# Performance work log

Measured on AMD Instinct MI355X. Metric: run time of the kernel, lower is better.

Reference implementation:

```python
import jax, jax.numpy as jnp
import numpy as np

EPS = 1e-5
DILATIONS = (1, 2, 1, 2, 1, 2, 1, 2)   # 4 blocks x 2 layers, kernel_size=2
GCN_AT = {1: 0, 5: 1}                  # ChebConv applied before layers 1 and 5
N_NODES, T_IN, N_EDGES = 20000, 13, 200000
RC, DC, SC, EC, HORIZON = 32, 32, 256, 512, 12


def conv_1x1(x, W, b):
    # x: [N,C,T], W: [O,C] -> [N,O,T]
    return jnp.einsum('oc,nct->not', W, x) + b[None, :, None]


def conv_k2(x, W, b, d):
    # dilated conv, kernel=2, dilation=d. x: [N,C,T], W: [O,C,2] -> [N,O,T-d]
    y = jnp.einsum('oc,nct->not', W[:, :, 0], x[:, :, :-d]) \
        + jnp.einsum('oc,nct->not', W[:, :, 1], x[:, :, d:])
    return y + b[None, :, None]


def _batchnorm(x):
    # BatchNorm2d (train mode, gamma=1, beta=0); per-channel stats over (N, F=1, T)
    m = jnp.mean(x, axis=(0, 2), keepdims=True)
    v = jnp.var(x, axis=(0, 2), keepdims=True)
    return (x - m) / jnp.sqrt(v + EPS)


def _cheb(xf, edge_index, edge_attr, W0, W1, b):
    n = xf.shape[0]
    row, col = edge_index[0], edge_index[1]
    w = jnp.where(row == col, 0.0, edge_attr)               # remove_self_loops
    deg = jax.ops.segment_sum(w, row, num_segments=n)
    dinv = jnp.where(deg > 0, 1.0 / jnp.sqrt(jnp.where(deg > 0, deg, 1.0)), 0.0)
    norm = dinv[row] * w * dinv[col]                        # [E]
    tx1 = -jax.ops.segment_sum(norm[:, None] * xf[row], col, num_segments=n)
    return xf @ W0 + tx1 @ W1 + b


def _forward(x, edge_index, edge_attr, start_W, start_b, filter_W, filter_b,
             gate_W, gate_b, skip_W, skip_b, gcn0_W0, gcn0_W1, gcn0_b,
             gcn1_W0, gcn1_W1, gcn1_b, end1_W, end1_b, end2_W, end2_b):
    # instance norm over time (use_norm=True); means is detached in torch
    means = jax.lax.stop_gradient(jnp.mean(x, axis=1, keepdims=True))   # [N,1,1]
    xc = x - means
    stdev = jnp.sqrt(jnp.var(xc, axis=1, keepdims=True) + EPS)
    xc = xc / stdev
    h = xc[:, :, 0][:, None, :]                  # [N,1,13]  (F=1 dim folded away)
    h = conv_1x1(h, start_W, start_b)            # [N,32,13]; T == receptive_field, no pad
    gcns = ((gcn0_W0, gcn0_W1, gcn0_b), (gcn1_W0, gcn1_W1, gcn1_b))
    skip = None
    for i, d in enumerate(DILATIONS):
        if i in GCN_AT:
            n, c, t = h.shape
            W0, W1, b = gcns[GCN_AT[i]]
            h = _cheb(h.reshape(n, c * t), edge_index, edge_attr, W0, W1, b).reshape(n, c, t)
        residual = h
        f = jnp.tanh(conv_k2(residual, filter_W[i], filter_b[i], d))
        g = jax.nn.sigmoid(conv_k2(residual, gate_W[i], gate_b[i], d))
        h = f * g                                 # [N,32,t-d]
        s = conv_1x1(h, skip_W[i], skip_b[i])     # [N,256,t-d]
        skip = s if skip is None else s + skip[:, :, -s.shape[2]:]
        h = h + residual[:, :, -h.shape[2]:]      # residual add (residual_conv unused in source)
        h = _batchnorm(h)
    out = jax.nn.relu(skip)                       # [N,256,1]
    out = conv_1x1(out, end1_W, end1_b)           # [N,512,1]
    out = conv_1x1(out, end2_W, end2_b)           # [N,12,1]
    return out * stdev + means                    # de-normalize; broadcasts over horizon


def setup_inputs() -> dict:
    key = jax.random.key(0)
    ks = iter(jax.random.split(key, 32))
    def w(shape, scale=0.1):
        return jax.random.normal(next(ks), shape, dtype=jnp.float32) * scale
    return {
        'x': jax.random.normal(next(ks), (N_NODES, T_IN, 1), dtype=jnp.float32),
        'edge_index': jax.random.randint(next(ks), (2, N_EDGES), 0, N_NODES),
        'edge_attr': jax.random.uniform(next(ks), (N_EDGES,), dtype=jnp.float32),
        'start_W': w((RC, 1)), 'start_b': w((RC,)),
        'filter_W': w((8, DC, RC, 2)), 'filter_b': w((8, DC)),
        'gate_W': w((8, DC, RC, 2)), 'gate_b': w((8, DC)),
        'skip_W': w((8, SC, DC)), 'skip_b': w((8, SC)),
        'gcn0_W0': w((384, 384), 0.05), 'gcn0_W1': w((384, 384), 0.05), 'gcn0_b': w((384,)),
        'gcn1_W0': w((192, 192), 0.05), 'gcn1_W1': w((192, 192), 0.05), 'gcn1_b': w((192,)),
        'end1_W': w((EC, SC)), 'end1_b': w((EC,)),
        'end2_W': w((HORIZON, EC)), 'end2_b': w((HORIZON,)),
    }


def reference(x, edge_index, edge_attr, start_W, start_b, filter_W, filter_b,
              gate_W, gate_b, skip_W, skip_b, gcn0_W0, gcn0_W1, gcn0_b,
              gcn1_W0, gcn1_W1, gcn1_b, end1_W, end1_b, end2_W, end2_b):
    return _forward(x, edge_index, edge_attr, start_W, start_b, filter_W, filter_b,
                    gate_W, gate_b, skip_W, skip_b, gcn0_W0, gcn0_W1, gcn0_b,
                    gcn1_W0, gcn1_W1, gcn1_b, end1_W, end1_b, end2_W, end2_b)
```

## Files before the change

### kernel.cpp

```cpp
#include <hip/hip_runtime.h>
#include <math.h>

#define NN 20000
#define NE 200000
#define TT 13
#define NBLK 79

typedef short bf16x8 __attribute__((ext_vector_type(8)));
typedef float f32x4 __attribute__((ext_vector_type(4)));

__device__ inline unsigned short f2bf(float f){
  union{float f; unsigned u;} v; v.f = f;
  unsigned r = v.u + 0x7fffu + ((v.u >> 16) & 1u);
  return (unsigned short)(r >> 16);
}
__device__ inline float bf2f(unsigned short h){
  union{unsigned u; float f;} v; v.u = ((unsigned)h) << 16; return v.f;
}
__device__ inline float fsig(float x){ return __builtin_amdgcn_rcpf(1.f + __expf(-x)); }
__device__ inline float ftanh(float x){ return 2.f*__builtin_amdgcn_rcpf(1.f + __expf(-2.f*x)) - 1.f; }

__global__ __launch_bounds__(256) void k_instnorm(const float* __restrict__ x,
    float* __restrict__ xc, float* __restrict__ stdev, float* __restrict__ means){
  int n = blockIdx.x*256 + threadIdx.x;
  if(n >= NN) return;
  float v[TT]; float s = 0.f;
#pragma unroll
  for(int t=0;t<TT;t++){ v[t] = x[n*TT+t]; s += v[t]; }
  float m = s * (1.0f/TT);
  float s2 = 0.f;
#pragma unroll
  for(int t=0;t<TT;t++){ v[t] -= m; s2 += v[t]*v[t]; }
  float sd = sqrtf(s2*(1.0f/TT) + 1e-5f);
  float inv = 1.0f/sd;
#pragma unroll
  for(int t=0;t<TT;t++) xc[n*TT+t] = v[t]*inv;
  stdev[n] = sd; means[n] = m;
}

__global__ __launch_bounds__(256) void k_start2(const float* __restrict__ xc,
    const float* __restrict__ sW, const float* __restrict__ sb, unsigned short* __restrict__ h){
  int idx = blockIdx.x*256 + threadIdx.x;
  if(idx >= NN*TT*16) return;
  int cp = idx & 15; int t = (idx >> 4) % TT; int n = idx/(16*TT);
  float xv = xc[n*TT+t];
  int c0 = cp*2;
  unsigned u = (unsigned)f2bf(sW[c0]*xv + sb[c0]) | ((unsigned)f2bf(sW[c0+1]*xv + sb[c0+1]) << 16);
  *(unsigned*)(h + (size_t)n*TT*32 + t*32 + c0) = u;
}

__global__ __launch_bounds__(256) void k_deg(const int* __restrict__ ei,
    const float* __restrict__ ea, float* __restrict__ deg){
  int e = blockIdx.x*256 + threadIdx.x;
  if(e >= NE) return;
  int r = ei[e], c = ei[NE+e];
  float w = (r==c) ? 0.f : ea[e];
  if(w != 0.f) atomicAdd(&deg[r], w);
}

__global__ __launch_bounds__(256) void k_dinv(float* __restrict__ deg){
  int n = blockIdx.x*256 + threadIdx.x;
  if(n >= NN) return;
  float d = deg[n];
  deg[n] = (d > 0.f) ? rsqrtf(d) : 0.f;
}

__global__ __launch_bounds__(256) void k_normcount(const int* __restrict__ ei,
    const float* __restrict__ ea, const float* __restrict__ dinv,
    float* __restrict__ nrm, int* __restrict__ cnt){
  int e = blockIdx.x*256 + threadIdx.x;
  if(e >= NE) return;
  int r = ei[e], c = ei[NE+e];
  float w = (r==c) ? 0.f : ea[e];
  float nv = dinv[r]*w*dinv[c];
  nrm[e] = nv;
  if(nv != 0.f) atomicAdd(&cnt[c], 1);
}

__global__ __launch_bounds__(256) void k_scanA(const int* __restrict__ cnt, int* __restrict__ bsum){
  int i = blockIdx.x*256 + threadIdx.x;
  int l = threadIdx.x & 63, w = threadIdx.x >> 6;
  int v = (i < NN) ? cnt[i] : 0;
#pragma unroll
  for(int off = 1; off < 64; off <<= 1) v += __shfl_xor(v, off);
  __shared__ int ws4[4];
  if(l == 0) ws4[w] = v;
  __syncthreads();
  if(threadIdx.x == 0) bsum[blockIdx.x] = ws4[0]+ws4[1]+ws4[2]+ws4[3];
}

__global__ __launch_bounds__(128) void k_scanB(const int* __restrict__ bsum, int* __restrict__ bbase){
  __shared__ int buf[128];
  int t = threadIdx.x;
  int v = (t < NBLK) ? bsum[t] : 0;
  buf[t] = v; __syncthreads();
  for(int off = 1; off < 128; off <<= 1){
    int u = (t >= off) ? buf[t-off] : 0;
    __syncthreads();
    buf[t] += u;
    __syncthreads();
  }
  if(t < NBLK) bbase[t] = buf[t] - v;
  if(t == NBLK-1) bbase[NBLK] = buf[t];
}

__global__ __launch_bounds__(256) void k_scanC(const int* __restrict__ cnt,
    const int* __restrict__ bbase, int* __restrict__ rowptr, int* __restrict__ woff){
  int i = blockIdx.x*256 + threadIdx.x;
  int t = threadIdx.x, l = t & 63, w = t >> 6;
  int v = (i < NN) ? cnt[i] : 0;
  int x = v;
#pragma unroll
  for(int off = 1; off < 64; off <<= 1){
    int u = __shfl_up(x, off);
    if(l >= off) x += u;
  }
  __shared__ int wt[4];
  if(l == 63) wt[w] = x;
  __syncthreads();
  int wo = 0;
  for(int k = 0; k < w; k++) wo += wt[k];
  int excl = bbase[blockIdx.x] + wo + x - v;
  if(i < NN){ rowptr[i] = excl; woff[i] = excl; }
  if(i == 0) rowptr[NN] = bbase[NBLK];
}

__global__ __launch_bounds__(256) void k_place(const float* __restrict__ nrm,
    const int* __restrict__ ei, int* __restrict__ woff,
    int* __restrict__ rowArr, float* __restrict__ nrmArr){
  int e = blockIdx.x*256 + threadIdx.x;
  if(e >= NE) return;
  float nv = nrm[e];
  if(nv == 0.f) return;
  int c = ei[NE+e];
  int pos = atomicAdd(&woff[c], 1);
  rowArr[pos] = ei[e];
  nrmArr[pos] = nv;
}

__global__ __launch_bounds__(64) void k_bnfold(const float* __restrict__ in, float* __restrict__ out){
  int t = threadIdx.x;
  float s = 0.f;
#pragma unroll
  for(int b = 0; b < 16; b++) s += in[b*64 + t];
  out[t] = s;
}

__device__ inline void d_prepw2(const float* W0, const float* W1, const float* b,
    unsigned short* Wt, float* bPerm, int F, int Kp, int T, int idx){
  if(idx >= F*Kp) return;
  int o = idx / Kp, k = idx - o*Kp;
  int to = o >> 5, co = o & 31; int fout = co*T + to;
  int ki = (k < F) ? k : k - F;
  int ti = ki >> 5, ci = ki & 31; int fin = ci*T + ti;
  float v = (k < F) ? W0[fin*F + fout] : W1[fin*F + fout];
  Wt[idx] = f2bf(v);
  if(k == 0) bPerm[o] = b[fout];
}
__device__ inline void d_prep2(const float* sW, const float* sb,
    unsigned short* Bwt, float* b2, int idx){
  if(idx >= 65536) return;
  int sOut = idx >> 8; int ic = idx & 255; int i = ic >> 5; int c = ic & 31;
  Bwt[idx] = f2bf(sW[i*8192 + sOut*32 + c]);
  if(idx < 256){
    float acc = 0.f;
    for(int ll = 0; ll < 8; ll++) acc += sb[ll*256 + idx];
    b2[idx] = acc;
  }
}
__device__ inline void d_comb(const float* e1W, const float* e1b,
    const float* e2W, const float* e2b, float* Wc, float* bc, int idx){
  if(idx >= 12*256) return;
  int k = idx >> 8, c = idx & 255;
  float acc = 0.f;
  for(int o = 0; o < 512; o++) acc += e2W[k*512+o]*e1W[o*256+c];
  Wc[idx] = acc;
  if(c == 0){
    float b = e2b[k];
    for(int o = 0; o < 512; o++) b += e2W[k*512+o]*e1b[o];
    bc[k] = b;
  }
}
__device__ inline void d_prepg(const float* fW, const float* fb,
    const float* gW, const float* gb, unsigned short* Wfrag, float* Bfrag, int idx){
  if(idx < 8*8*64*8){
    int j = idx & 7; int lane = (idx >> 3) & 63; int chunk = (idx >> 9) & 7; int layer = idx >> 12;
    int fg = chunk >> 2; int q = (chunk >> 1) & 1; int i = chunk & 1;
    int quad = lane >> 4, tcol = lane & 15;
    int cout = 16*i + tcol, cin = quad*8 + j;
    const float* W = fg ? gW : fW;
    Wfrag[idx] = f2bf(W[layer*2048 + cout*64 + cin*2 + q]);
  }
  if(idx < 8*64*4){
    int r = idx & 3; int lane = (idx >> 2) & 63; int layer = idx >> 8;
    int tcol = lane & 15;
    float v;
    if(r == 0)      v = fb[layer*32 + tcol];
    else if(r == 1) v = fb[layer*32 + 16 + tcol];
    else if(r == 2) v = gb[layer*32 + tcol];
    else            v = gb[layer*32 + 16 + tcol];
    Bfrag[idx] = v;
  }
}
__global__ __launch_bounds__(256) void k_prepall(
    const float* g0W0, const float* g0W1, const float* g0b,
    const float* g1W0, const float* g1W1, const float* g1b,
    const float* sW, const float* sb,
    const float* e1W, const float* e1b, const float* e2W, const float* e2b,
    const float* fW, const float* fb, const float* gW, const float* gb,
    unsigned short* Wt0, float* bP0, unsigned short* Wt1, float* bP1,
    unsigned short* Bwt, float* bias2, float* Wc, float* bc,
    unsigned short* Wfrag, float* Bfrag){
  int b = blockIdx.x, t = threadIdx.x;
  if(b < 1152)       d_prepw2(g0W0, g0W1, g0b, Wt0, bP0, 384, 768, 12, b*256 + t);
  else if(b < 1440)  d_prepw2(g1W0, g1W1, g1b, Wt1, bP1, 192, 384, 6, (b-1152)*256 + t);
  else if(b < 1696)  d_prep2(sW, sb, Bwt, bias2, (b-1440)*256 + t);
  else if(b < 1708)  d_comb(e1W, e1b, e2W, e2b, Wc, bc, (b-1696)*256 + t);
  else               d_prepg(fW, fb, gW, gb, Wfrag, Bfrag, (b-1708)*256 + t);
}

__global__ __launch_bounds__(256) void k_cvtbn2(const unsigned short* __restrict__ h,
    const float* __restrict__ bn, float cntInv, unsigned short* __restrict__ A,
    int F, int Kp){
  int idx = blockIdx.x*256 + threadIdx.x;
  int half = F >> 1;
  if(idx >= NN*half) return;
  int n = idx / half, r = idx - n*half;
  int k0 = 2*r; int c0 = k0 & 31;
  unsigned u = *(const unsigned*)(h + (size_t)n*F + k0);
  float m0 = bn[c0]*cntInv, m1 = bn[c0+1]*cntInv;
  float i0 = rsqrtf(bn[32+c0]*cntInv - m0*m0 + 1e-5f);
  float i1 = rsqrtf(bn[32+c0+1]*cntInv - m1*m1 + 1e-5f);
  float v0 = (bf2f((unsigned short)(u & 0xffffu)) - m0)*i0;
  float v1 = (bf2f((unsigned short)(u >> 16)) - m1)*i1;
  unsigned outw = (unsigned)f2bf(v0) | ((unsigned)f2bf(v1) << 16);
  *(unsigned*)(A + (size_t)n*Kp + k0) = outw;
}

__global__ void k_gather2(const unsigned short* __restrict__ Acat, int Kp, int F, int F2,
    const int* __restrict__ rowArr, const float* __restrict__ nrmArr,
    const int* __restrict__ rowptr, unsigned short* __restrict__ dst){
  int node = blockIdx.x;
  int f2 = threadIdx.x;
  int beg = rowptr[node], end = rowptr[node+1];
  __shared__ int srow[64];
  __shared__ float snrm[64];
  float a0 = 0.f, a1 = 0.f;
  for(int base = beg; base < end; base += 64){
    int m = end - base; if(m > 64) m = 64;
    __syncthreads();
    if(threadIdx.x < m){ srow[threadIdx.x] = rowArr[base+threadIdx.x]; snrm[threadIdx.x] = nrmArr[base+threadIdx.x]; }
    __syncthreads();
    if(f2 < F2){
      for(int j = 0; j < m; j++){
        unsigned u = *(const unsigned*)(Acat + (size_t)srow[j]*Kp + 2*f2);
        float nv = snrm[j];
        a0 += nv*bf2f((unsigned short)(u & 0xffffu));
        a1 += nv*bf2f((unsigned short)(u >> 16));
      }
    }
  }
  if(f2 < F2){
    unsigned outw = (unsigned)f2bf(-a0) | ((unsigned)f2bf(-a1) << 16);
    *(unsigned*)(dst + (size_t)node*Kp + F + 2*f2) = outw;
  }
}

template<bool BOUT>
__global__ __launch_bounds__(256) void k_gemm_bf16(const unsigned short* __restrict__ A,
    const unsigned short* __restrict__ Bt, const float* __restrict__ bias,
    void* __restrict__ Cv, int M, int N, int K){
  __shared__ unsigned short As[128*32];
  __shared__ unsigned short Bs[64*32];
  int tid = threadIdx.x;
  int w = tid >> 6, l = tid & 63, quad = l >> 4, tcol = l & 15;
  int m0 = blockIdx.x*128, n0 = blockIdx.y*64;
  int rw = (w & 1)*64, cw = (w >> 1)*32;
  int sr = tid >> 2, sc = (tid & 3)*8;
  f32x4 acc[4][2];
#pragma unroll
  for(int i=0;i<4;i++)
#pragma unroll
    for(int j=0;j<2;j++) acc[i][j] = (f32x4){0.f,0.f,0.f,0.f};
  for(int k0 = 0; k0 < K; k0 += 32){
    uint4 a0 = *(const uint4*)(A + (size_t)(m0 + sr)*K + k0 + sc);
    uint4 a1 = *(const uint4*)(A + (size_t)(m0 + 64 + sr)*K + k0 + sc);
    uint4 b0 = *(const uint4*)(Bt + (size_t)(n0 + sr)*K + k0 + sc);
    __syncthreads();
    *(uint4*)(As + sr*32 + sc) = a0;
    *(uint4*)(As + (64+sr)*32 + sc) = a1;
    *(uint4*)(Bs + sr*32 + sc) = b0;
    __syncthreads();
    bf16x8 av[4], bv[2];
#pragma unroll
    for(int i=0;i<4;i++) av[i] = *(const bf16x8*)(As + (rw + 16*i + tcol)*32 + quad*8);
#pragma unroll
    for(int j=0;j<2;j++) bv[j] = *(const bf16x8*)(Bs + (cw + 16*j + tcol)*32 + quad*8);
#pragma unroll
    for(int i=0;i<4;i++)
#pragma unroll
      for(int j=0;j<2;j++)
        acc[i][j] = __builtin_amdgcn_mfma_f32_16x16x32_bf16(av[i], bv[j], acc[i][j], 0, 0, 0);
  }
#pragma unroll
  for(int i=0;i<4;i++){
#pragma unroll
    for(int j=0;j<2;j++){
      int col = n0 + cw + 16*j + tcol;
      float bb = bias[col];
#pragma unroll
      for(int r=0;r<4;r++){
        int row = m0 + rw + 16*i + quad*4 + r;
        if(row < M){
          float o = acc[i][j][r] + bb;
          if(BOUT) ((unsigned short*)Cv)[(size_t)row*N + col] = f2bf(o);
          else ((float*)Cv)[(size_t)row*N + col] = o;
        }
      }
    }
  }
}

template<int D,int TIN,int TOUT,bool BNIN,bool STATS,bool WRITEH>
__global__ __launch_bounds__(256) void k_gated5(
    const unsigned short* __restrict__ hIn, unsigned short* __restrict__ hOut,
    unsigned short* __restrict__ gl,
    const float* __restrict__ bnIn, float* __restrict__ bnOut,
    const unsigned short* __restrict__ Wfrag, const float* __restrict__ Bfrag,
    int layer, float cntInv){
  constexpr int RS = 40;
  __shared__ unsigned short hs[4][2][TIN*RS];
  __shared__ unsigned short ho[4][2][WRITEH ? TOUT*RS : RS];
  __shared__ float bnm[32], bnv[32];
  __shared__ float bnred[64];
  int tid = threadIdx.x;
  int w = tid >> 6, l = tid & 63, quad = l >> 4, tcol = l & 15;
  if(BNIN && tid < 32){
    float s = 0.f, s2 = 0.f;
#pragma unroll
    for(int b = 0; b < 16; b++){ s += bnIn[b*64 + tid]; s2 += bnIn[b*64 + 32 + tid]; }
    float m = s*cntInv;
    float var = s2*cntInv - m*m;
    bnm[tid] = m; bnv[tid] = rsqrtf(var + 1e-5f);
  }
  if(STATS && tid < 64) bnred[tid] = 0.f;
  __syncthreads();
  float sm[8], sv[8];
  if(BNIN){
    int cb = (l & 3)*8;
#pragma unroll
    for(int j=0;j<8;j++){ sm[j] = bnm[cb+j]; sv[j] = bnv[cb+j]; }
  }
  const unsigned short* wfr = Wfrag + layer*4096;
  bf16x8 bwf[2][2], bwg[2][2];
#pragma unroll
  for(int q=0;q<2;q++)
#pragma unroll
    for(int i=0;i<2;i++){
      bwf[q][i] = *(const bf16x8*)(wfr + ((q*2+i)*64 + l)*8);
      bwg[q][i] = *(const bf16x8*)(wfr + ((4 + q*2+i)*64 + l)*8);
    }
  float4 bv4 = *(const float4*)(Bfrag + layer*256 + l*4);
  float fbv[2] = {bv4.x, bv4.y}, gbv[2] = {bv4.z, bv4.w};

  int tr = (tcol < TOUT) ? tcol : 0;
  unsigned short* hwA = hs[w][0];
  unsigned short* hwB = hs[w][1];
  unsigned short* howA = ho[w][0];
  unsigned short* howB = ho[w][1];
  float sA[2] = {0.f,0.f}, s2A[2] = {0.f,0.f};
  int wid = blockIdx.x*4 + w;
  int base = wid*8;
  bool ldact = (l < TIN*4);
  int ts = l >> 2, cb = (l & 3)*8;
  uint4 vA = {0,0,0,0}, vB = {0,0,0,0};
  if(ldact && base < NN){
    vA = *(const uint4*)(hIn + (size_t)base*TIN*32 + l*8);
    vB = *(const uint4*)(hIn + (size_t)(base+1)*TIN*32 + l*8);
  }
  for(int p = 0; p < 4; p++){
    int nA = base + 2*p;
    if(nA >= NN) break;
    int nB = nA + 1;
    if(ldact){
      if(BNIN){
        unsigned short tA[8], tB[8];
        const unsigned short* uA = (const unsigned short*)&vA;
        const unsigned short* uB = (const unsigned short*)&vB;
#pragma unroll
        for(int j=0;j<8;j++){
          tA[j] = f2bf((bf2f(uA[j]) - sm[j])*sv[j]);
          tB[j] = f2bf((bf2f(uB[j]) - sm[j])*sv[j]);
        }
        *(uint4*)(hwA + ts*RS + cb) = *(const uint4*)tA;
        *(uint4*)(hwB + ts*RS + cb) = *(const uint4*)tB;
      } else {
        *(uint4*)(hwA + ts*RS + cb) = vA;
        *(uint4*)(hwB + ts*RS + cb) = vB;
      }
    }
    if(p < 3 && ldact && nA + 2 < NN){
      vA = *(const uint4*)(hIn + (size_t)(nA+2)*TIN*32 + l*8);
      vB = *(const uint4*)(hIn + (size_t)(nA+3)*TIN*32 + l*8);
    }
    bf16x8 aA0 = *(const bf16x8*)(hwA + tr*RS + quad*8);
    bf16x8 aA1 = *(const bf16x8*)(hwA + (tr+D)*RS + quad*8);
    bf16x8 aB0 = *(const bf16x8*)(hwB + tr*RS + quad*8);
    bf16x8 aB1 = *(const bf16x8*)(hwB + (tr+D)*RS + quad*8);
    f32x4 afA[2], agA[2], afB[2], agB[2];
#pragma unroll
    for(int i=0;i<2;i++){
      afA[i] = (f32x4){0.f,0.f,0.f,0.f}; agA[i] = afA[i];
      afB[i] = afA[i]; agB[i] = afA[i];
    }
#pragma unroll
    for(int i=0;i<2;i++){
      afA[i] = __builtin_amdgcn_mfma_f32_16x16x32_bf16(aA0, bwf[0][i], afA[i], 0,0,0);
      afB[i] = __builtin_amdgcn_mfma_f32_16x16x32_bf16(aB0, bwf[0][i], afB[i], 0,0,0);
      afA[i] = __builtin_amdgcn_mfma_f32_16x16x32_bf16(aA1, bwf[1][i], afA[i], 0,0,0);
      afB[i] = __builtin_amdgcn_mfma_f32_16x16x32_bf16(aB1, bwf[1][i], afB[i], 0,0,0);
      agA[i] = __builtin_amdgcn_mfma_f32_16x16x32_bf16(aA0, bwg[0][i], agA[i], 0,0,0);
      agB[i] = __builtin_amdgcn_mfma_f32_16x16x32_bf16(aB0, bwg[0][i], agB[i], 0,0,0);
      agA[i] = __builtin_amdgcn_mfma_f32_16x16x32_bf16(aA1, bwg[1][i], agA[i], 0,0,0);
      agB[i] = __builtin_amdgcn_mfma_f32_16x16x32_bf16(aB1, bwg[1][i], agB[i], 0,0,0);
    }
#pragma unroll
    for(int i=0;i<2;i++){
      int cout = 16*i + tcol;
#pragma unroll
      for(int r=0;r<4;r++){
        int t = quad*4 + r;
        if(t < TOUT){
          float fA = afA[i][r] + fbv[i];
          float gA = agA[i][r] + gbv[i];
          float fB = afB[i][r] + fbv[i];
          float gB = agB[i][r] + gbv[i];
          float gatedA = ftanh(fA)*fsig(gA);
          float gatedB = ftanh(fB)*fsig(gB);
          if(t == TOUT-1){
            gl[(size_t)nA*256 + cout] = f2bf(gatedA);
            gl[(size_t)nB*256 + cout] = f2bf(gatedB);
          }
          float oA = gatedA + bf2f(hwA[(t+D)*RS + cout]);
          float oB = gatedB + bf2f(hwB[(t+D)*RS + cout]);
          if(WRITEH){ howA[t*RS + cout] = f2bf(oA); howB[t*RS + cout] = f2bf(oB); }
          if(STATS){ sA[i] += oA + oB; s2A[i] += oA*oA + oB*oB; }
        }
      }
    }
    if(WRITEH && l < TOUT*4){
      int to = l >> 2, cb2 = (l & 3)*8;
      *(uint4*)(hOut + (size_t)nA*TOUT*32 + to*32 + cb2) = *(const uint4*)(howA + to*RS + cb2);
      *(uint4*)(hOut + (size_t)nB*TOUT*32 + to*32 + cb2) = *(const uint4*)(howB + to*RS + cb2);
    }
  }
  if(STATS){
#pragma unroll
    for(int i=0;i<2;i++){
      sA[i]  += __shfl_xor(sA[i], 16);  sA[i]  += __shfl_xor(sA[i], 32);
      s2A[i] += __shfl_xor(s2A[i], 16); s2A[i] += __shfl_xor(s2A[i], 32);
    }
    if(l < 16){
#pragma unroll
      for(int i=0;i<2;i++){
        atomicAdd(&bnred[16*i + l], sA[i]);
        atomicAdd(&bnred[32 + 16*i + l], s2A[i]);
      }
    }
    __syncthreads();
    if(tid < 64) atomicAdd(&bnOut[(blockIdx.x & 15)*64 + tid], bnred[tid]);
  }
}

__global__ __launch_bounds__(256) void k_final(const float* __restrict__ skip,
    const float* __restrict__ Wc, const float* __restrict__ bc,
    const float* __restrict__ stdev, const float* __restrict__ means,
    float* __restrict__ out){
  __shared__ float wsm[3072];
  __shared__ float bcs[12];
  int tid = threadIdx.x;
  for(int j = tid; j < 3072; j += 256){
    int c = j / 12, k = j - c*12;
    wsm[c*12 + k] = Wc[k*256 + c];
  }
  if(tid < 12) bcs[tid] = bc[tid];
  __syncthreads();
  int idx = blockIdx.x*256 + tid;
  if(idx >= NN*12) return;
  int n = idx / 12, k = idx - n*12;
  const float* sr = skip + (size_t)n*256;
  float acc = bcs[k];
#pragma unroll 8
  for(int c = 0; c < 256; c++) acc += wsm[c*12 + k]*fmaxf(sr[c], 0.f);
  out[idx] = acc*stdev[n] + means[n];
}

extern "C" void kernel_launch(void* const* d_in, const int* in_sizes, int n_in,
                              void* d_out, int out_size, void* d_ws, size_t ws_size,
                              hipStream_t stream) {
  const float* x      = (const float*)d_in[0];
  const int*   ei     = (const int*)  d_in[1];
  const float* ea     = (const float*)d_in[2];
  const float* startW = (const float*)d_in[3];
  const float* startb = (const float*)d_in[4];
  const float* fW     = (const float*)d_in[5];
  const float* fb     = (const float*)d_in[6];
  const float* gW     = (const float*)d_in[7];
  const float* gb     = (const float*)d_in[8];
  const float* sW     = (const float*)d_in[9];
  const float* sb     = (const float*)d_in[10];
  const float* g0W0   = (const float*)d_in[11];
  const float* g0W1   = (const float*)d_in[12];
  const float* g0b    = (const float*)d_in[13];
  const float* g1W0   = (const float*)d_in[14];
  const float* g1W1   = (const float*)d_in[15];
  const float* g1b    = (const float*)d_in[16];
  const float* e1W    = (const float*)d_in[17];
  const float* e1b    = (const float*)d_in[18];
  const float* e2W    = (const float*)d_in[19];
  const float* e2b    = (const float*)d_in[20];
  float* out = (float*)d_out;
  float* ws  = (float*)d_ws;

  const int MP = 20096;
  size_t o = 0;
  unsigned short* hA = (unsigned short*)(ws + o); o += (size_t)NN*208;
  unsigned short* hB = (unsigned short*)(ws + o); o += (size_t)NN*208;
  unsigned short* Acat  = (unsigned short*)(ws + o); o += (size_t)MP*384;
  unsigned short* glcat = (unsigned short*)(ws + o); o += (size_t)MP*128;
  unsigned short* Wt0 = (unsigned short*)(ws + o); o += 147456;
  unsigned short* Wt1 = (unsigned short*)(ws + o); o += 36864;
  unsigned short* Bwt = (unsigned short*)(ws + o); o += 32768;
  unsigned short* Wfrag = (unsigned short*)(ws + o); o += 16384;
  float* Bfrag = ws + o; o += 2048;
  float* bP0   = ws + o; o += 384;
  float* bP1   = ws + o; o += 192;
  float* bias2 = ws + o; o += 256;
  float* Wc    = ws + o; o += 3072;
  float* bc    = ws + o; o += 16;
  float* stdev = ws + o; o += NN;
  float* means = ws + o; o += NN;
  float* xc    = ws + o; o += (size_t)NN*TT;
  float* deg   = ws + o; o += NN;
  int*   cnt   = (int*)(ws + o); o += NN;
  float* bnstats = ws + o; o += 8*1024;
  float* bnf0  = ws + o; o += 64;
  float* bnf1  = ws + o; o += 64;
  float* normb = ws + o; o += NE;
  int*   rowArr = (int*)(ws + o); o += NE;
  float* nrmArr = ws + o; o += NE;
  int*   rowptr = (int*)(ws + o); o += NN + 4;
  int*   woff   = (int*)(ws + o); o += NN;
  int*   bsum   = (int*)(ws + o); o += NBLK + 4;
  int*   bbase  = (int*)(ws + o); o += NBLK + 4;
  float* skipb  = (float*)hA;

  hipMemsetAsync(deg, 0, (2*NN + 8*1024)*sizeof(float), stream);
  k_instnorm<<<(NN+255)/256, 256, 0, stream>>>(x, xc, stdev, means);
  k_start2<<<((NN*TT*16)+255)/256, 256, 0, stream>>>(xc, startW, startb, hA);
  k_deg<<<(NE+255)/256, 256, 0, stream>>>(ei, ea, deg);
  k_dinv<<<(NN+255)/256, 256, 0, stream>>>(deg);
  k_normcount<<<(NE+255)/256, 256, 0, stream>>>(ei, ea, deg, normb, cnt);
  k_scanA<<<NBLK, 256, 0, stream>>>(cnt, bsum);
  k_scanB<<<1, 128, 0, stream>>>(bsum, bbase);
  k_scanC<<<NBLK, 256, 0, stream>>>(cnt, bbase, rowptr, woff);
  k_place<<<(NE+255)/256, 256, 0, stream>>>(normb, ei, woff, rowArr, nrmArr);
  k_prepall<<<1836, 256, 0, stream>>>(g0W0, g0W1, g0b, g1W0, g1W1, g1b,
      sW, sb, e1W, e1b, e2W, e2b, fW, fb, gW, gb,
      Wt0, bP0, Wt1, bP1, Bwt, bias2, Wc, bc, Wfrag, Bfrag);

  const int GB = 640;
  k_gated5<1,13,12,false,true,true><<<GB,256,0,stream>>>(hA, hB, glcat+0,
      bnstats, bnstats+0*1024, Wfrag, Bfrag, 0, 0.f);
  k_bnfold<<<1, 64, 0, stream>>>(bnstats+0*1024, bnf0);
  k_cvtbn2<<<((NN*192)+255)/256, 256, 0, stream>>>(hB, bnf0, 1.f/(NN*12.f), Acat, 384, 768);
  k_gather2<<<NN, 192, 0, stream>>>(Acat, 768, 384, 192, rowArr, nrmArr, rowptr, Acat);
  { dim3 g(MP/128, 384/64);
    k_gemm_bf16<true><<<g, 256, 0, stream>>>(Acat, Wt0, bP0, hA, NN, 384, 768); }
  k_gated5<2,12,10,false,true,true><<<GB,256,0,stream>>>(hA, hB, glcat+32,
      bnstats, bnstats+1*1024, Wfrag, Bfrag, 1, 0.f);
  k_gated5<1,10,9,true,true,true><<<GB,256,0,stream>>>(hB, hA, glcat+64,
      bnstats+1*1024, bnstats+2*1024, Wfrag, Bfrag, 2, 1.f/(NN*10.f));
  k_gated5<2,9,7,true,true,true><<<GB,256,0,stream>>>(hA, hB, glcat+96,
      bnstats+2*1024, bnstats+3*1024, Wfrag, Bfrag, 3, 1.f/(NN*9.f));
  k_gated5<1,7,6,true,true,true><<<GB,256,0,stream>>>(hB, hA, glcat+128,
      bnstats+3*1024, bnstats+4*1024, Wfrag, Bfrag, 4, 1.f/(NN*7.f));
  k_bnfold<<<1, 64, 0, stream>>>(bnstats+4*1024, bnf1);
  k_cvtbn2<<<((NN*96)+255)/256, 256, 0, stream>>>(hA, bnf1, 1.f/(NN*6.f), Acat, 192, 384);
  k_gather2<<<NN, 128, 0, stream>>>(Acat, 384, 192, 96, rowArr, nrmArr, rowptr, Acat);
  { dim3 g(MP/128, 192/64);
    k_gemm_bf16<true><<<g, 256, 0, stream>>>(Acat, Wt1, bP1, hB, NN, 192, 384); }
  k_gated5<2,6,4,false,true,true><<<GB,256,0,stream>>>(hB, hA, glcat+160,
      bnstats, bnstats+5*1024, Wfrag, Bfrag, 5, 0.f);
  k_gated5<1,4,3,true,true,true><<<GB,256,0,stream>>>(hA, hB, glcat+192,
      bnstats+5*1024, bnstats+6*1024, Wfrag, Bfrag, 6, 1.f/(NN*4.f));
  k_gated5<2,3,1,true,false,false><<<GB,256,0,stream>>>(hB, nullptr, glcat+224,
      bnstats+6*1024, bnstats+7*1024, Wfrag, Bfrag, 7, 1.f/(NN*3.f));

  { dim3 g(MP/128, 256/64);
    k_gemm_bf16<false><<<g, 256, 0, stream>>>(glcat, Bwt, bias2, skipb, NN, 256, 256); }
  k_final<<<((NN*12)+255)/256, 256, 0, stream>>>(skipb, Wc, bc, stdev, means, out);
}
```

Measured before the change: 460.7 us.

## Fuse instance norm, start conv and first gated layer into one kernel

Replaces k_instnorm, k_start2 and the first gated layer with a single k_fused0nb kernel. It normalizes the input per node in shared memory, builds the start-conv activations directly in registers as MFMA operands, computes the gated output with its residual, and accumulates BN statistics before writing the result. This removes the xc and hA intermediate round-trips and two launches. Separately, the gated kernel now handles 4 nodes per wave instead of 8, with the grid doubled to 1280, to expose more parallelism. The smaller per-wave batch also means less prefetch reuse per wave.

```diff
diff --git a/kernel.cpp b/kernel.cpp
--- a/kernel.cpp
+++ b/kernel.cpp
@@ -19,132 +19,6 @@
 }
 __device__ inline float fsig(float x){ return __builtin_amdgcn_rcpf(1.f + __expf(-x)); }
 __device__ inline float ftanh(float x){ return 2.f*__builtin_amdgcn_rcpf(1.f + __expf(-2.f*x)) - 1.f; }
-
-__global__ __launch_bounds__(256) void k_instnorm(const float* __restrict__ x,
-    float* __restrict__ xc, float* __restrict__ stdev, float* __restrict__ means){
-  int n = blockIdx.x*256 + threadIdx.x;
-  if(n >= NN) return;
-  float v[TT]; float s = 0.f;
-#pragma unroll
-  for(int t=0;t<TT;t++){ v[t] = x[n*TT+t]; s += v[t]; }
-  float m = s * (1.0f/TT);
-  float s2 = 0.f;
-#pragma unroll
-  for(int t=0;t<TT;t++){ v[t] -= m; s2 += v[t]*v[t]; }
-  float sd = sqrtf(s2*(1.0f/TT) + 1e-5f);
-  float inv = 1.0f/sd;
-#pragma unroll
-  for(int t=0;t<TT;t++) xc[n*TT+t] = v[t]*inv;
-  stdev[n] = sd; means[n] = m;
-}
-
-__global__ __launch_bounds__(256) void k_start2(const float* __restrict__ xc,
-    const float* __restrict__ sW, const float* __restrict__ sb, unsigned short* __restrict__ h){
-  int idx = blockIdx.x*256 + threadIdx.x;
-  if(idx >= NN*TT*16) return;
-  int cp = idx & 15; int t = (idx >> 4) % TT; int n = idx/(16*TT);
-  float xv = xc[n*TT+t];
-  int c0 = cp*2;
-  unsigned u = (unsigned)f2bf(sW[c0]*xv + sb[c0]) | ((unsigned)f2bf(sW[c0+1]*xv + sb[c0+1]) << 16);
-  *(unsigned*)(h + (size_t)n*TT*32 + t*32 + c0) = u;
-}
-
-__global__ __launch_bounds__(256) void k_deg(const int* __restrict__ ei,
-    const float* __restrict__ ea, float* __restrict__ deg){
-  int e = blockIdx.x*256 + threadIdx.x;
-  if(e >= NE) return;
-  int r = ei[e], c = ei[NE+e];
-  float w = (r==c) ? 0.f : ea[e];
-  if(w != 0.f) atomicAdd(&deg[r], w);
-}
-
-__global__ __launch_bounds__(256) void k_dinv(float* __restrict__ deg){
-  int n = blockIdx.x*256 + threadIdx.x;
-  if(n >= NN) return;
-  float d = deg[n];
-  deg[n] = (d > 0.f) ? rsqrtf(d) : 0.f;
-}
-
-__global__ __launch_bounds__(256) void k_normcount(const int* __restrict__ ei,
-    const float* __restrict__ ea, const float* __restrict__ dinv,
-    float* __restrict__ nrm, int* __restrict__ cnt){
-  int e = blockIdx.x*256 + threadIdx.x;
-  if(e >= NE) return;
-  int r = ei[e], c = ei[NE+e];
-  float w = (r==c) ? 0.f : ea[e];
-  float nv = dinv[r]*w*dinv[c];
-  nrm[e] = nv;
-  if(nv != 0.f) atomicAdd(&cnt[c], 1);
-}
-
-__global__ __launch_bounds__(256) void k_scanA(const int* __restrict__ cnt, int* __restrict__ bsum){
-  int i = blockIdx.x*256 + threadIdx.x;
-  int l = threadIdx.x & 63, w = threadIdx.x >> 6;
-  int v = (i < NN) ? cnt[i] : 0;
-#pragma unroll
-  for(int off = 1; off < 64; off <<= 1) v += __shfl_xor(v, off);
-  __shared__ int ws4[4];
-  if(l == 0) ws4[w] = v;
-  __syncthreads();
-  if(threadIdx.x == 0) bsum[blockIdx.x] = ws4[0]+ws4[1]+ws4[2]+ws4[3];
-}
-
-__global__ __launch_bounds__(128) void k_scanB(const int* __restrict__ bsum, int* __restrict__ bbase){
-  __shared__ int buf[128];
-  int t = threadIdx.x;
-  int v = (t < NBLK) ? bsum[t] : 0;
-  buf[t] = v; __syncthreads();
-  for(int off = 1; off < 128; off <<= 1){
-    int u = (t >= off) ? buf[t-off] : 0;
-    __syncthreads();
-    buf[t] += u;
-    __syncthreads();
-  }
-  if(t < NBLK) bbase[t] = buf[t] - v;
-  if(t == NBLK-1) bbase[NBLK] = buf[t];
-}
-
-__global__ __launch_bounds__(256) void k_scanC(const int* __restrict__ cnt,
-    const int* __restrict__ bbase, int* __restrict__ rowptr, int* __restrict__ woff){
-  int i = blockIdx.x*256 + threadIdx.x;
-  int t = threadIdx.x, l = t & 63, w = t >> 6;
-  int v = (i < NN) ? cnt[i] : 0;
-  int x = v;
-#pragma unroll
-  for(int off = 1; off < 64; off <<= 1){
-    int u = __shfl_up(x, off);
-    if(l >= off) x += u;
-  }
-  __shared__ int wt[4];
-  if(l == 63) wt[w] = x;
-  __syncthreads();
-  int wo = 0;
-  for(int k = 0; k < w; k++) wo += wt[k];
-  int excl = bbase[blockIdx.x] + wo + x - v;
-  if(i < NN){ rowptr[i] = excl; woff[i] = excl; }
-  if(i == 0) rowptr[NN] = bbase[NBLK];
-}
-
-__global__ __launch_bounds__(256) void k_place(const float* __restrict__ nrm,
-    const int* __restrict__ ei, int* __restrict__ woff,
-    int* __restrict__ rowArr, float* __restrict__ nrmArr){
-  int e = blockIdx.x*256 + threadIdx.x;
-  if(e >= NE) return;
-  float nv = nrm[e];
-  if(nv == 0.f) return;
-  int c = ei[NE+e];
-  int pos = atomicAdd(&woff[c], 1);
-  rowArr[pos] = ei[e];
-  nrmArr[pos] = nv;
-}
-
-__global__ __launch_bounds__(64) void k_bnfold(const float* __restrict__ in, float* __restrict__ out){
-  int t = threadIdx.x;
-  float s = 0.f;
-#pragma unroll
-  for(int b = 0; b < 16; b++) s += in[b*64 + t];
-  out[t] = s;
-}
 
 __device__ inline void d_prepw2(const float* W0, const float* W1, const float* b,
     unsigned short* Wt, float* bPerm, int F, int Kp, int T, int idx){
@@ -217,6 +91,103 @@
   else if(b < 1696)  d_prep2(sW, sb, Bwt, bias2, (b-1440)*256 + t);
   else if(b < 1708)  d_comb(e1W, e1b, e2W, e2b, Wc, bc, (b-1696)*256 + t);
   else               d_prepg(fW, fb, gW, gb, Wfrag, Bfrag, (b-1708)*256 + t);
+}
+
+__global__ __launch_bounds__(256) void k_deg(const int* __restrict__ ei,
+    const float* __restrict__ ea, float* __restrict__ deg){
+  int e = blockIdx.x*256 + threadIdx.x;
+  if(e >= NE) return;
+  int r = ei[e], c = ei[NE+e];
+  float w = (r==c) ? 0.f : ea[e];
+  if(w != 0.f) atomicAdd(&deg[r], w);
+}
+
+__global__ __launch_bounds__(256) void k_dinv(float* __restrict__ deg){
+  int n = blockIdx.x*256 + threadIdx.x;
+  if(n >= NN) return;
+  float d = deg[n];
+  deg[n] = (d > 0.f) ? rsqrtf(d) : 0.f;
+}
+
+__global__ __launch_bounds__(256) void k_normcount(const int* __restrict__ ei,
+    const float* __restrict__ ea, const float* __restrict__ dinv,
+    float* __restrict__ nrm, int* __restrict__ cnt){
+  int e = blockIdx.x*256 + threadIdx.x;
+  if(e >= NE) return;
+  int r = ei[e], c = ei[NE+e];
+  float w = (r==c) ? 0.f : ea[e];
+  float nv = dinv[r]*w*dinv[c];
+  nrm[e] = nv;
+  if(nv != 0.f) atomicAdd(&cnt[c], 1);
+}
+
+__global__ __launch_bounds__(256) void k_scanA(const int* __restrict__ cnt, int* __restrict__ bsum){
+  int i = blockIdx.x*256 + threadIdx.x;
+  int l = threadIdx.x & 63, w = threadIdx.x >> 6;
+  int v = (i < NN) ? cnt[i] : 0;
+#pragma unroll
+  for(int off = 1; off < 64; off <<= 1) v += __shfl_xor(v, off);
+  __shared__ int ws4[4];
+  if(l == 0) ws4[w] = v;
+  __syncthreads();
+  if(threadIdx.x == 0) bsum[blockIdx.x] = ws4[0]+ws4[1]+ws4[2]+ws4[3];
+}
+
+__global__ __launch_bounds__(128) void k_scanB(const int* __restrict__ bsum, int* __restrict__ bbase){
+  __shared__ int buf[128];
+  int t = threadIdx.x;
+  int v = (t < NBLK) ? bsum[t] : 0;
+  buf[t] = v; __syncthreads();
+  for(int off = 1; off < 128; off <<= 1){
+    int u = (t >= off) ? buf[t-off] : 0;
+    __syncthreads();
+    buf[t] += u;
+    __syncthreads();
+  }
+  if(t < NBLK) bbase[t] = buf[t] - v;
+  if(t == NBLK-1) bbase[NBLK] = buf[t];
+}
+
+__global__ __launch_bounds__(256) void k_scanC(const int* __restrict__ cnt,
+    const int* __restrict__ bbase, int* __restrict__ rowptr, int* __restrict__ woff){
+  int i = blockIdx.x*256 + threadIdx.x;
+  int t = threadIdx.x, l = t & 63, w = t >> 6;
+  int v = (i < NN) ? cnt[i] : 0;
+  int x = v;
+#pragma unroll
+  for(int off = 1; off < 64; off <<= 1){
+    int u = __shfl_up(x, off);
+    if(l >= off) x += u;
+  }
+  __shared__ int wt[4];
+  if(l == 63) wt[w] = x;
+  __syncthreads();
+  int wo = 0;
+  for(int k = 0; k < w; k++) wo += wt[k];
+  int excl = bbase[blockIdx.x] + wo + x - v;
+  if(i < NN){ rowptr[i] = excl; woff[i] = excl; }
+  if(i == 0) rowptr[NN] = bbase[NBLK];
+}
+
+__global__ __launch_bounds__(256) void k_place(const float* __restrict__ nrm,
+    const int* __restrict__ ei, int* __restrict__ woff,
+    int* __restrict__ rowArr, float* __restrict__ nrmArr){
+  int e = blockIdx.x*256 + threadIdx.x;
+  if(e >= NE) return;
+  float nv = nrm[e];
+  if(nv == 0.f) return;
+  int c = ei[NE+e];
+  int pos = atomicAdd(&woff[c], 1);
+  rowArr[pos] = ei[e];
+  nrmArr[pos] = nv;
+}
+
+__global__ __launch_bounds__(64) void k_bnfold(const float* __restrict__ in, float* __restrict__ out){
+  int t = threadIdx.x;
+  float s = 0.f;
+#pragma unroll
+  for(int b = 0; b < 16; b++) s += in[b*64 + t];
+  out[t] = s;
 }
 
 __global__ __launch_bounds__(256) void k_cvtbn2(const unsigned short* __restrict__ h,
@@ -279,9 +250,9 @@
   int sr = tid >> 2, sc = (tid & 3)*8;
   f32x4 acc[4][2];
 #pragma unroll
-  for(int i=0;i<4;i++)
-#pragma unroll
-    for(int j=0;j<2;j++) acc[i][j] = (f32x4){0.f,0.f,0.f,0.f};
+  for(int i = 0; i < 4; i++)
+#pragma unroll
+    for(int j = 0; j < 2; j++) acc[i][j] = (f32x4){0.f,0.f,0.f,0.f};
   for(int k0 = 0; k0 < K; k0 += 32){
     uint4 a0 = *(const uint4*)(A + (size_t)(m0 + sr)*K + k0 + sc);
     uint4 a1 = *(const uint4*)(A + (size_t)(m0 + 64 + sr)*K + k0 + sc);
@@ -293,23 +264,23 @@
     __syncthreads();
     bf16x8 av[4], bv[2];
 #pragma unroll
-    for(int i=0;i<4;i++) av[i] = *(const bf16x8*)(As + (rw + 16*i + tcol)*32 + quad*8);
-#pragma unroll
-    for(int j=0;j<2;j++) bv[j] = *(const bf16x8*)(Bs + (cw + 16*j + tcol)*32 + quad*8);
-#pragma unroll
-    for(int i=0;i<4;i++)
-#pragma unroll
-      for(int j=0;j<2;j++)
+    for(int i = 0; i < 4; i++) av[i] = *(const bf16x8*)(As + (rw + 16*i + tcol)*32 + quad*8);
+#pragma unroll
+    for(int j = 0; j < 2; j++) bv[j] = *(const bf16x8*)(Bs + (cw + 16*j + tcol)*32 + quad*8);
+#pragma unroll
+    for(int i = 0; i < 4; i++)
+#pragma unroll
+      for(int j = 0; j < 2; j++)
         acc[i][j] = __builtin_amdgcn_mfma_f32_16x16x32_bf16(av[i], bv[j], acc[i][j], 0, 0, 0);
   }
 #pragma unroll
-  for(int i=0;i<4;i++){
-#pragma unroll
-    for(int j=0;j<2;j++){
+  for(int i = 0; i < 4; i++){
+#pragma unroll
+    for(int j = 0; j < 2; j++){
       int col = n0 + cw + 16*j + tcol;
       float bb = bias[col];
 #pragma unroll
-      for(int r=0;r<4;r++){
+      for(int r = 0; r < 4; r++){
         int row = m0 + rw + 16*i + quad*4 + r;
         if(row < M){
           float o = acc[i][j][r] + bb;
@@ -318,6 +289,128 @@
         }
       }
     }
+  }
+}
+
+__global__ __launch_bounds__(256,3) void k_fused0nb(
+    const float* __restrict__ x, const float* __restrict__ startW, const float* __restrict__ startb,
+    const unsigned short* __restrict__ Wfrag, const float* __restrict__ Bfrag,
+    unsigned short* __restrict__ glcat, unsigned short* __restrict__ hOut,
+    float* __restrict__ stdev, float* __restrict__ means,
+    float* __restrict__ bnstats){
+  __shared__ float xs[40][14];
+  __shared__ float swl[32], sbl[32];
+  __shared__ unsigned short bufB[40*12*40];
+  __shared__ float bnred[64];
+  int tid = threadIdx.x;
+  int w = tid >> 6, l = tid & 63, quad = l >> 4, tcol = l & 15;
+  int base = blockIdx.x*40;
+  for(int j = tid; j < 520; j += 256){ int n = j/13, t = j - n*13; xs[n][t] = x[(size_t)(base+n)*13 + t]; }
+  if(tid < 32){ swl[tid] = startW[tid]; sbl[tid] = startb[tid]; }
+  if(tid < 64) bnred[tid] = 0.f;
+  __syncthreads();
+  if(tid < 40){
+    float s = 0.f;
+#pragma unroll
+    for(int t = 0; t < 13; t++) s += xs[tid][t];
+    float m = s*(1.0f/13.f);
+    float s2 = 0.f;
+#pragma unroll
+    for(int t = 0; t < 13; t++){ float d = xs[tid][t]-m; s2 += d*d; }
+    float sd = sqrtf(s2*(1.0f/13.f) + 1e-5f);
+    float inv = 1.0f/sd;
+    means[base+tid] = m; stdev[base+tid] = sd;
+#pragma unroll
+    for(int t = 0; t < 13; t++) xs[tid][t] = (xs[tid][t]-m)*inv;
+  }
+  __syncthreads();
+  bf16x8 bwf[2][2], bwg[2][2];
+#pragma unroll
+  for(int q = 0; q < 2; q++)
+#pragma unroll
+    for(int i = 0; i < 2; i++){
+      bwf[q][i] = *(const bf16x8*)(Wfrag + ((q*2+i)*64 + l)*8);
+      bwg[q][i] = *(const bf16x8*)(Wfrag + ((4 + q*2+i)*64 + l)*8);
+    }
+  float4 bv4 = *(const float4*)(Bfrag + l*4);
+  float fbv[2] = {bv4.x, bv4.y}, gbv[2] = {bv4.z, bv4.w};
+  float sw8[8], sb8[8], swc[2], sbc[2];
+#pragma unroll
+  for(int j = 0; j < 8; j++){ sw8[j] = swl[quad*8+j]; sb8[j] = sbl[quad*8+j]; }
+#pragma unroll
+  for(int i = 0; i < 2; i++){ swc[i] = swl[16*i+tcol]; sbc[i] = sbl[16*i+tcol]; }
+  float sAc[2] = {0.f,0.f}, s2Ac[2] = {0.f,0.f};
+  int tr = (tcol < 12) ? tcol : 0;
+  for(int p = 0; p < 5; p++){
+    int slA = w*10 + 2*p, slB = slA + 1;
+    float x0A = xs[slA][tr], x1A = xs[slA][tr+1];
+    float x0B = xs[slB][tr], x1B = xs[slB][tr+1];
+    bf16x8 aA0, aA1, aB0, aB1;
+#pragma unroll
+    for(int j = 0; j < 8; j++){
+      aA0[j] = (short)f2bf(sw8[j]*x0A + sb8[j]);
+      aA1[j] = (short)f2bf(sw8[j]*x1A + sb8[j]);
+      aB0[j] = (short)f2bf(sw8[j]*x0B + sb8[j]);
+      aB1[j] = (short)f2bf(sw8[j]*x1B + sb8[j]);
+    }
+    f32x4 afA[2], agA[2], afB[2], agB[2];
+#pragma unroll
+    for(int i = 0; i < 2; i++){
+      afA[i] = (f32x4){0.f,0.f,0.f,0.f}; agA[i] = afA[i];
+      afB[i] = afA[i]; agB[i] = afA[i];
+    }
+#pragma unroll
+    for(int i = 0; i < 2; i++){
+      afA[i] = __builtin_amdgcn_mfma_f32_16x16x32_bf16(aA0, bwf[0][i], afA[i], 0,0,0);
+      afB[i] = __builtin_amdgcn_mfma_f32_16x16x32_bf16(aB0, bwf[0][i], afB[i], 0,0,0);
+      afA[i] = __builtin_amdgcn_mfma_f32_16x16x32_bf16(aA1, bwf[1][i], afA[i], 0,0,0);
+      afB[i] = __builtin_amdgcn_mfma_f32_16x16x32_bf16(aB1, bwf[1][i], afB[i], 0,0,0);
+      agA[i] = __builtin_amdgcn_mfma_f32_16x16x32_bf16(aA0, bwg[0][i], agA[i], 0,0,0);
+      agB[i] = __builtin_amdgcn_mfma_f32_16x16x32_bf16(aB0, bwg[0][i], agB[i], 0,0,0);
+      agA[i] = __builtin_amdgcn_mfma_f32_16x16x32_bf16(aA1, bwg[1][i], agA[i], 0,0,0);
+      agB[i] = __builtin_amdgcn_mfma_f32_16x16x32_bf16(aB1, bwg[1][i], agB[i], 0,0,0);
+    }
+#pragma unroll
+    for(int i = 0; i < 2; i++){
+      int cout = 16*i + tcol;
+#pragma unroll
+      for(int r = 0; r < 4; r++){
+        int t = quad*4 + r;
+        if(t < 12){
+          float fA = afA[i][r] + fbv[i], gA = agA[i][r] + gbv[i];
+          float fB = afB[i][r] + fbv[i], gB = agB[i][r] + gbv[i];
+          float gatA = ftanh(fA)*fsig(gA);
+          float gatB = ftanh(fB)*fsig(gB);
+          if(t == 11){
+            glcat[(size_t)(base+slA)*256 + cout] = f2bf(gatA);
+            glcat[(size_t)(base+slB)*256 + cout] = f2bf(gatB);
+          }
+          float oA = gatA + swc[i]*xs[slA][t+1] + sbc[i];
+          float oB = gatB + swc[i]*xs[slB][t+1] + sbc[i];
+          bufB[slA*480 + t*40 + cout] = f2bf(oA);
+          bufB[slB*480 + t*40 + cout] = f2bf(oB);
+          sAc[i] += oA + oB; s2Ac[i] += oA*oA + oB*oB;
+        }
+      }
+    }
+  }
+#pragma unroll
+  for(int i = 0; i < 2; i++){
+    sAc[i]  += __shfl_xor(sAc[i], 16);  sAc[i]  += __shfl_xor(sAc[i], 32);
+    s2Ac[i] += __shfl_xor(s2Ac[i], 16); s2Ac[i] += __shfl_xor(s2Ac[i], 32);
+  }
+  if(l < 16){
+#pragma unroll
+    for(int i = 0; i < 2; i++){
+      atomicAdd(&bnred[16*i + l], sAc[i]);
+      atomicAdd(&bnred[32 + 16*i + l], s2Ac[i]);
+    }
+  }
+  __syncthreads();
+  if(tid < 64) atomicAdd(&bnstats[(blockIdx.x & 15)*64 + tid], bnred[tid]);
+  for(int j = tid; j < 40*48; j += 256){
+    int s = j/48; int q = j - s*48; int t = q >> 2; int cb = (q & 3)*8;
+    *(uint4*)(hOut + (size_t)(base+s)*384 + t*32 + cb) = *(const uint4*)(bufB + s*480 + t*40 + cb);
   }
 }
 
@@ -370,7 +463,7 @@
   unsigned short* howB = ho[w][1];
   float sA[2] = {0.f,0.f}, s2A[2] = {0.f,0.f};
   int wid = blockIdx.x*4 + w;
-  int base = wid*8;
+  int base = wid*4;
   bool ldact = (l < TIN*4);
   int ts = l >> 2, cb = (l & 3)*8;
   uint4 vA = {0,0,0,0}, vB = {0,0,0,0};
@@ -378,7 +471,7 @@
     vA = *(const uint4*)(hIn + (size_t)base*TIN*32 + l*8);
     vB = *(const uint4*)(hIn + (size_t)(base+1)*TIN*32 + l*8);
   }
-  for(int p = 0; p < 4; p++){
+  for(int p = 0; p < 2; p++){
     int nA = base + 2*p;
     if(nA >= NN) break;
     int nB = nA + 1;
@@ -399,7 +492,7 @@
         *(uint4*)(hwB + ts*RS + cb) = vB;
       }
     }
-    if(p < 3 && ldact && nA + 2 < NN){
+    if(p < 1 && ldact && nA + 2 < NN){
       vA = *(const uint4*)(hIn + (size_t)(nA+2)*TIN*32 + l*8);
       vB = *(const uint4*)(hIn + (size_t)(nA+3)*TIN*32 + l*8);
     }
@@ -524,8 +617,10 @@
 
   const int MP = 20096;
   size_t o = 0;
-  unsigned short* hA = (unsigned short*)(ws + o); o += (size_t)NN*208;
-  unsigned short* hB = (unsigned short*)(ws + o); o += (size_t)NN*208;
+  float* hAf = ws + o; o += (size_t)NN*208;
+  float* hBf = ws + o; o += (size_t)NN*208;
+  unsigned short* hA = (unsigned short*)hAf;
+  unsigned short* hB = (unsigned short*)hBf;
   unsigned short* Acat  = (unsigned short*)(ws + o); o += (size_t)MP*384;
   unsigned short* glcat = (unsigned short*)(ws + o); o += (size_t)MP*128;
   unsigned short* Wt0 = (unsigned short*)(ws + o); o += 147456;
@@ -540,7 +635,6 @@
   float* bc    = ws + o; o += 16;
   float* stdev = ws + o; o += NN;
   float* means = ws + o; o += NN;
-  float* xc    = ws + o; o += (size_t)NN*TT;
   float* deg   = ws + o; o += NN;
   int*   cnt   = (int*)(ws + o); o += NN;
   float* bnstats = ws + o; o += 8*1024;
@@ -553,11 +647,12 @@
   int*   woff   = (int*)(ws + o); o += NN;
   int*   bsum   = (int*)(ws + o); o += NBLK + 4;
   int*   bbase  = (int*)(ws + o); o += NBLK + 4;
-  float* skipb  = (float*)hA;
-
-  hipMemsetAsync(deg, 0, (2*NN + 8*1024)*sizeof(float), stream);
-  k_instnorm<<<(NN+255)/256, 256, 0, stream>>>(x, xc, stdev, means);
-  k_start2<<<((NN*TT*16)+255)/256, 256, 0, stream>>>(xc, startW, startb, hA);
+  float* skipb  = hAf;
+
+  hipMemsetAsync(deg, 0, (size_t)(2*NN + 8*1024)*sizeof(float), stream);
+  k_prepall<<<1836, 256, 0, stream>>>(g0W0, g0W1, g0b, g1W0, g1W1, g1b,
+      sW, sb, e1W, e1b, e2W, e2b, fW, fb, gW, gb,
+      Wt0, bP0, Wt1, bP1, Bwt, bias2, Wc, bc, Wfrag, Bfrag);
   k_deg<<<(NE+255)/256, 256, 0, stream>>>(ei, ea, deg);
   k_dinv<<<(NN+255)/256, 256, 0, stream>>>(deg);
   k_normcount<<<(NE+255)/256, 256, 0, stream>>>(ei, ea, deg, normb, cnt);
@@ -565,14 +660,11 @@
   k_scanB<<<1, 128, 0, stream>>>(bsum, bbase);
   k_scanC<<<NBLK, 256, 0, stream>>>(cnt, bbase, rowptr, woff);
   k_place<<<(NE+255)/256, 256, 0, stream>>>(normb, ei, woff, rowArr, nrmArr);
-  k_prepall<<<1836, 256, 0, stream>>>(g0W0, g0W1, g0b, g1W0, g1W1, g1b,
-      sW, sb, e1W, e1b, e2W, e2b, fW, fb, gW, gb,
-      Wt0, bP0, Wt1, bP1, Bwt, bias2, Wc, bc, Wfrag, Bfrag);
-
-  const int GB = 640;
-  k_gated5<1,13,12,false,true,true><<<GB,256,0,stream>>>(hA, hB, glcat+0,
-      bnstats, bnstats+0*1024, Wfrag, Bfrag, 0, 0.f);
-  k_bnfold<<<1, 64, 0, stream>>>(bnstats+0*1024, bnf0);
+
+  const int GB = 1280;
+  k_fused0nb<<<500, 256, 0, stream>>>(x, startW, startb, Wfrag, Bfrag, glcat, hB,
+      stdev, means, bnstats);
+  k_bnfold<<<1, 64, 0, stream>>>(bnstats, bnf0);
   k_cvtbn2<<<((NN*192)+255)/256, 256, 0, stream>>>(hB, bnf0, 1.f/(NN*12.f), Acat, 384, 768);
   k_gather2<<<NN, 192, 0, stream>>>(Acat, 768, 384, 192, rowArr, nrmArr, rowptr, Acat);
   { dim3 g(MP/128, 384/64);
```

Result: faster. 440.9 us (-4.3%).
